# Kernel optimization log

Measured on AMD Instinct MI355X. Metric: run time of the kernel, lower is better.

## Reference

```python
import jax, jax.numpy as jnp
import numpy as np


def squash(v, axis=-1):
    # scale = |v|^2 / (1+|v|^2) / |v|, applied elementwise along `axis`
    s2 = jnp.sum(jnp.square(v), axis=axis, keepdims=True)
    scale = s2 / (1.0 + s2) / jnp.sqrt(s2)
    return scale * v


def setup_inputs() -> dict:
    key = jax.random.key(0)
    k1, k2 = jax.random.split(key)
    B, I, D_in = 128, 1152, 8   # batch, input_num_capsule, input_dim_vector
    N, D_out = 32, 16           # num_capsule, dim_vector
    inputs = jax.random.normal(k1, (B, I, D_in), dtype=jnp.float32)
    # glorot_uniform-like scale for W: [in_caps, num_caps, in_dim, out_dim]
    limit = np.sqrt(6.0 / (D_in + D_out)).astype(np.float32)
    W = jax.random.uniform(k2, (I, N, D_in, D_out), dtype=jnp.float32,
                           minval=-limit, maxval=limit)
    bias = jnp.zeros((1, I, N), dtype=jnp.float32)  # routing logits (zeros init)
    return {"inputs": inputs, "W": W, "bias": bias}


def reference(inputs, W, bias):
    num_routing = 3
    # inputs_hat[b,i,n,e] = sum_d inputs[b,i,d] * W[i,n,d,e]
    # (the original's tf.scan over batch + batch_dot is just this einsum)
    u_hat = jnp.einsum('bid,inde->bine', inputs, W)  # [B,I,N,E]

    b = jnp.broadcast_to(bias, u_hat.shape[:3])  # [B,I,N] (bias broadcasts over batch)
    outputs = None
    for it in range(num_routing):
        c = jax.nn.softmax(b, axis=2)                       # softmax over num_capsule
        s = jnp.einsum('bin,bine->bne', c, u_hat)           # weighted sum over in_caps
        outputs = squash(s, axis=-1)                        # [B,N,E]
        if it != num_routing - 1:
            # agreement update: b += <u_hat, v>
            b = b + jnp.einsum('bine,bne->bin', u_hat, outputs)
    return outputs  # [B, num_capsule, dim_vector]
```

## Files before the change

kernel.cpp:

```cpp
#include <hip/hip_runtime.h>
#include <hip/hip_fp16.h>

namespace {

constexpr int kB = 128, kI = 1152, kD = 8, kN = 32, kE = 16;
constexpr int kTI = 4;
constexpr int kNC = kI / kTI;
constexpr int kCG = 4;
constexpr int kCPG = kNC / kCG;

constexpr size_t kPartBytes = (size_t)kNC * kB * kN * kE * 2;
constexpr size_t kPart2Bytes = (size_t)kCG * kB * kN * kE * 4;
constexpr size_t kVsumBytes = (size_t)kB * kN * kE * 4;

typedef _Float16 h2v __attribute__((ext_vector_type(2)));

__device__ __forceinline__ float fdot2(__half2 a, __half2 b, float c) {
#if defined(__has_builtin) && __has_builtin(__builtin_amdgcn_fdot2)
  return __builtin_amdgcn_fdot2(__builtin_bit_cast(h2v, a),
                                __builtin_bit_cast(h2v, b), c, false);
#else
  float2 af = __half22float2(a), bf = __half22float2(b);
  return fmaf(af.y, bf.y, fmaf(af.x, bf.x, c));
#endif
}

union I4H { int4 v; __half2 h[4]; };

template<int PASS>
__global__ __launch_bounds__(256, 2)
void caps_pass(const float* __restrict__ x, const float* __restrict__ W,
               const float* __restrict__ bias, const __half* __restrict__ vsh,
               __half* __restrict__ part)
{
  __shared__ __half2 wlds[kTI * kD * 64 * 4];
  __shared__ __half2 xlds[32][kTI * kD];

  const int chunk = (int)blockIdx.x;
  const int i0 = chunk * kTI;
  const int b0 = (int)blockIdx.y * 32;
  const int t = (int)threadIdx.x;
  const int lane = t & 63;
  const int wv = t >> 6;
  const int eh = lane >> 5;
  const int n  = lane & 31;

  {
    const float2* wsrc = reinterpret_cast<const float2*>(
        W + (size_t)chunk * (kTI * kN * kD * kE));
    const int e  = (t * 2) & 15;
    const int dd = ((t * 2) >> 4) & 7;
    const int ehw = e >> 3, ep = (e & 7) >> 1;
#pragma unroll
    for (int iter = 0; iter < 32; ++iter) {
      const int nn_i = iter * 4 + (t >> 6);
      const int nn = nn_i & 31, ii = nn_i >> 5;
      float2 f2 = wsrc[iter * 256 + t];
      wlds[((ii * kD + dd) * 64 + ehw * 32 + nn) * 4 + ep] =
          __floats2half2_rn(f2.x, f2.y);
    }
  }
  {
    const int r = t >> 3, c = (t & 7) * 4;
    const float4 f4 = *reinterpret_cast<const float4*>(
        x + (size_t)(b0 + r) * (kI * kD) + i0 * kD + c);
    xlds[r][c + 0] = __half2half2(__float2half_rn(f4.x));
    xlds[r][c + 1] = __half2half2(__float2half_rn(f4.y));
    xlds[r][c + 2] = __half2half2(__float2half_rn(f4.z));
    xlds[r][c + 3] = __half2half2(__float2half_rn(f4.w));
  }
  __syncthreads();

  __half2 wr[kTI][kD][4];
#pragma unroll
  for (int i = 0; i < kTI; ++i)
#pragma unroll
    for (int d = 0; d < kD; ++d) {
      I4H q; q.v = *reinterpret_cast<const int4*>(&wlds[((i * kD + d) * 64 + lane) * 4]);
#pragma unroll
      for (int k = 0; k < 4; ++k) wr[i][d][k] = q.h[k];
    }

  float bf[kTI];
#pragma unroll
  for (int i = 0; i < kTI; ++i) bf[i] = bias[(size_t)(i0 + i) * kN + n];

  __half2 c0[kTI];
  if (PASS == 0) {
#pragma unroll
    for (int i = 0; i < kTI; ++i) {
      float lg = bf[i];
      float m = lg;
#pragma unroll
      for (int o = 1; o <= 16; o <<= 1) m = fmaxf(m, __shfl_xor(m, o, 64));
      float ev = __expf(lg - m);
      float sm = ev;
#pragma unroll
      for (int o = 1; o <= 16; o <<= 1) sm += __shfl_xor(sm, o, 64);
      c0[i] = __half2half2(__float2half_rn(ev / sm));
    }
  }

#pragma unroll 2
  for (int bb = 0; bb < 8; ++bb) {
    const int bl = wv * 8 + bb;
    const int b = b0 + bl;
    I4H vq;
    if (PASS > 0)
      vq.v = *reinterpret_cast<const int4*>(vsh + ((size_t)b * kN + n) * kE + eh * 8);

    __half2 s[4];
#pragma unroll
    for (int k = 0; k < 4; ++k) s[k] = __half2half2(__float2half(0.f));

#pragma unroll
    for (int i = 0; i < kTI; ++i) {
      I4H xa, xb;
      xa.v = *reinterpret_cast<const int4*>(&xlds[bl][i * kD]);
      xb.v = *reinterpret_cast<const int4*>(&xlds[bl][i * kD + 4]);
      __half2 uh[4];
#pragma unroll
      for (int k = 0; k < 4; ++k) uh[k] = __hmul2(xa.h[0], wr[i][0][k]);
#pragma unroll
      for (int d = 1; d < 4; ++d)
#pragma unroll
        for (int k = 0; k < 4; ++k) uh[k] = __hfma2(xa.h[d], wr[i][d][k], uh[k]);
#pragma unroll
      for (int d = 0; d < 4; ++d)
#pragma unroll
        for (int k = 0; k < 4; ++k) uh[k] = __hfma2(xb.h[d], wr[i][4 + d][k], uh[k]);

      __half2 c2;
      if (PASS == 0) {
        c2 = c0[i];
      } else {
        float lg = bf[i];
#pragma unroll
        for (int k = 0; k < 4; ++k) lg = fdot2(uh[k], vq.h[k], lg);
        lg += __shfl_xor(lg, 32, 64);
        float m = lg;
#pragma unroll
        for (int o = 1; o <= 16; o <<= 1) m = fmaxf(m, __shfl_xor(m, o, 64));
        float ev = __expf(lg - m);
        float sm = ev;
#pragma unroll
        for (int o = 1; o <= 16; o <<= 1) sm += __shfl_xor(sm, o, 64);
        c2 = __half2half2(__float2half_rn(ev / sm));
      }
#pragma unroll
      for (int k = 0; k < 4; ++k) s[k] = __hfma2(c2, uh[k], s[k]);
    }
    I4H o;
#pragma unroll
    for (int k = 0; k < 4; ++k) o.h[k] = s[k];
    *reinterpret_cast<int4*>(
        part + (((size_t)chunk * kB + b) * kN + n) * kE + eh * 8) = o.v;
  }
}

__global__ __launch_bounds__(256)
void caps_reduce1(const __half* __restrict__ part, float* __restrict__ partial2)
{
  const int b = (int)blockIdx.x, cg = (int)blockIdx.y;
  const int t = (int)threadIdx.x;
  const int nl = t >> 3, ep = t & 7;
  const __half2* p = reinterpret_cast<const __half2*>(
      part + (((size_t)(cg * kCPG) * kB + b) * kN + nl) * kE + ep * 2);
  const size_t stride = (size_t)kB * kN * kE / 2;
  float ax = 0.f, ay = 0.f;
#pragma unroll 8
  for (int ch = 0; ch < kCPG; ++ch) {
    float2 f = __half22float2(p[(size_t)ch * stride]);
    ax += f.x; ay += f.y;
  }
  *reinterpret_cast<float2*>(
      partial2 + (((size_t)cg * kB + b) * kN + nl) * kE + ep * 2) = make_float2(ax, ay);
}

template<int MODE>
__global__ __launch_bounds__(256)
void caps_final(const float* __restrict__ partial2, float* __restrict__ vsum,
                __half* __restrict__ vsh, float* __restrict__ out)
{
  const int b = (int)blockIdx.x;
  const int t = (int)threadIdx.x;
  const int nl = t >> 3, ep = t & 7;
  const size_t o = ((size_t)b * kN + nl) * kE + ep * 2;
  float ax = 0.f, ay = 0.f;
#pragma unroll
  for (int cg = 0; cg < kCG; ++cg) {
    float2 f = *reinterpret_cast<const float2*>(
        partial2 + (size_t)cg * kB * kN * kE + o);
    ax += f.x; ay += f.y;
  }
  float s2 = ax * ax + ay * ay;
  s2 += __shfl_xor(s2, 1, 64);
  s2 += __shfl_xor(s2, 2, 64);
  s2 += __shfl_xor(s2, 4, 64);
  const float sc = (s2 / (1.f + s2)) * rsqrtf(fmaxf(s2, 1e-30f));
  float vx = ax * sc, vy = ay * sc;
  if (MODE == 2) {
    *reinterpret_cast<float2*>(out + o) = make_float2(vx, vy);
  } else {
    if (MODE == 1) {
      float2 old = *reinterpret_cast<const float2*>(vsum + o);
      vx += old.x; vy += old.y;
    }
    *reinterpret_cast<float2*>(vsum + o) = make_float2(vx, vy);
    *reinterpret_cast<__half2*>(vsh + o) = __floats2half2_rn(vx, vy);
  }
}

}

extern "C" void kernel_launch(void* const* d_in, const int* in_sizes, int n_in,
                              void* d_out, int out_size, void* d_ws, size_t ws_size,
                              hipStream_t stream) {
  (void)in_sizes; (void)n_in; (void)out_size; (void)ws_size;
  const float* x    = reinterpret_cast<const float*>(d_in[0]);
  const float* W    = reinterpret_cast<const float*>(d_in[1]);
  const float* bias = reinterpret_cast<const float*>(d_in[2]);
  float* out = reinterpret_cast<float*>(d_out);

  char* ws = reinterpret_cast<char*>(d_ws);
  __half* part     = reinterpret_cast<__half*>(ws);
  float*  partial2 = reinterpret_cast<float*>(ws + kPartBytes);
  float*  vsum     = reinterpret_cast<float*>(ws + kPartBytes + kPart2Bytes);
  __half* vsh      = reinterpret_cast<__half*>(ws + kPartBytes + kPart2Bytes + kVsumBytes);

  dim3 pg(kNC, kB / 32), pb(256);
  dim3 rg(kB, kCG), rb(256);

  caps_pass<0><<<pg, pb, 0, stream>>>(x, W, bias, vsh, part);
  caps_reduce1<<<rg, rb, 0, stream>>>(part, partial2);
  caps_final<0><<<kB, 256, 0, stream>>>(partial2, vsum, vsh, out);
  caps_pass<1><<<pg, pb, 0, stream>>>(x, W, bias, vsh, part);
  caps_reduce1<<<rg, rb, 0, stream>>>(part, partial2);
  caps_final<1><<<kB, 256, 0, stream>>>(partial2, vsum, vsh, out);
  caps_pass<2><<<pg, pb, 0, stream>>>(x, W, bias, vsh, part);
  caps_reduce1<<<rg, rb, 0, stream>>>(part, partial2);
  caps_final<2><<<kB, 256, 0, stream>>>(partial2, vsum, vsh, out);
}
```

Baseline: 204.9 us.

## Load W directly into registers and widen reduction loads to 16 bytes

The pass kernel drops the LDS staging buffer for W. Each thread now reads its own W slice from global memory straight into registers with float4 loads, which removes the shared-memory round trip and about 32 KB of LDS per block. The only barrier left guards the x tile. The reduce kernel is restructured so each thread accumulates 8 halves through 128-bit loads, with 4 batches per block and a quarter of the blocks. The risk is less coalesced W global reads, since lanes stride by n across 512 B rows.

```diff
diff --git a/kernel.cpp b/kernel.cpp
--- a/kernel.cpp
+++ b/kernel.cpp
@@ -9,9 +9,9 @@
 constexpr int kCG = 4;
 constexpr int kCPG = kNC / kCG;
 
-constexpr size_t kPartBytes = (size_t)kNC * kB * kN * kE * 2;
+constexpr size_t kPartBytes  = (size_t)kNC * kB * kN * kE * 2;
 constexpr size_t kPart2Bytes = (size_t)kCG * kB * kN * kE * 4;
-constexpr size_t kVsumBytes = (size_t)kB * kN * kE * 4;
+constexpr size_t kVsumBytes  = (size_t)kB * kN * kE * 4;
 
 typedef _Float16 h2v __attribute__((ext_vector_type(2)));
 
@@ -33,7 +33,6 @@
                const float* __restrict__ bias, const __half* __restrict__ vsh,
                __half* __restrict__ part)
 {
-  __shared__ __half2 wlds[kTI * kD * 64 * 4];
   __shared__ __half2 xlds[32][kTI * kD];
 
   const int chunk = (int)blockIdx.x;
@@ -46,40 +45,31 @@
   const int n  = lane & 31;
 
   {
-    const float2* wsrc = reinterpret_cast<const float2*>(
-        W + (size_t)chunk * (kTI * kN * kD * kE));
-    const int e  = (t * 2) & 15;
-    const int dd = ((t * 2) >> 4) & 7;
-    const int ehw = e >> 3, ep = (e & 7) >> 1;
-#pragma unroll
-    for (int iter = 0; iter < 32; ++iter) {
-      const int nn_i = iter * 4 + (t >> 6);
-      const int nn = nn_i & 31, ii = nn_i >> 5;
-      float2 f2 = wsrc[iter * 256 + t];
-      wlds[((ii * kD + dd) * 64 + ehw * 32 + nn) * 4 + ep] =
-          __floats2half2_rn(f2.x, f2.y);
-    }
-  }
-  {
     const int r = t >> 3, c = (t & 7) * 4;
     const float4 f4 = *reinterpret_cast<const float4*>(
-        x + (size_t)(b0 + r) * (kI * kD) + i0 * kD + c);
+        x + (size_t)(b0 + r) * (kI * kD) + (size_t)i0 * kD + c);
     xlds[r][c + 0] = __half2half2(__float2half_rn(f4.x));
     xlds[r][c + 1] = __half2half2(__float2half_rn(f4.y));
     xlds[r][c + 2] = __half2half2(__float2half_rn(f4.z));
     xlds[r][c + 3] = __half2half2(__float2half_rn(f4.w));
   }
-  __syncthreads();
 
   __half2 wr[kTI][kD][4];
-#pragma unroll
-  for (int i = 0; i < kTI; ++i)
-#pragma unroll
-    for (int d = 0; d < kD; ++d) {
-      I4H q; q.v = *reinterpret_cast<const int4*>(&wlds[((i * kD + d) * 64 + lane) * 4]);
-#pragma unroll
-      for (int k = 0; k < 4; ++k) wr[i][d][k] = q.h[k];
-    }
+  {
+    const float* wb = W + ((size_t)i0 * kN + n) * (kD * kE) + eh * 8;
+#pragma unroll
+    for (int i = 0; i < kTI; ++i)
+#pragma unroll
+      for (int d = 0; d < kD; ++d) {
+        const float4* p = reinterpret_cast<const float4*>(
+            wb + (size_t)i * (kN * kD * kE) + d * kE);
+        float4 a = p[0], b4 = p[1];
+        wr[i][d][0] = __floats2half2_rn(a.x, a.y);
+        wr[i][d][1] = __floats2half2_rn(a.z, a.w);
+        wr[i][d][2] = __floats2half2_rn(b4.x, b4.y);
+        wr[i][d][3] = __floats2half2_rn(b4.z, b4.w);
+      }
+  }
 
   float bf[kTI];
 #pragma unroll
@@ -100,6 +90,8 @@
       c0[i] = __half2half2(__float2half_rn(ev / sm));
     }
   }
+
+  __syncthreads();
 
 #pragma unroll 2
   for (int bb = 0; bb < 8; ++bb) {
@@ -161,20 +153,25 @@
 __global__ __launch_bounds__(256)
 void caps_reduce1(const __half* __restrict__ part, float* __restrict__ partial2)
 {
-  const int b = (int)blockIdx.x, cg = (int)blockIdx.y;
+  const int cg = (int)blockIdx.y;
   const int t = (int)threadIdx.x;
-  const int nl = t >> 3, ep = t & 7;
-  const __half2* p = reinterpret_cast<const __half2*>(
-      part + (((size_t)(cg * kCPG) * kB + b) * kN + nl) * kE + ep * 2);
-  const size_t stride = (size_t)kB * kN * kE / 2;
-  float ax = 0.f, ay = 0.f;
-#pragma unroll 8
+  const int b = (int)blockIdx.x * 4 + (t >> 6);
+  const int l = t & 63;
+  const __half* p0 = part + ((size_t)(cg * kCPG) * kB + b) * (kN * kE) + l * 8;
+  constexpr size_t chStride = (size_t)kB * kN * kE;
+  float acc[8] = {0.f, 0.f, 0.f, 0.f, 0.f, 0.f, 0.f, 0.f};
+#pragma unroll 4
   for (int ch = 0; ch < kCPG; ++ch) {
-    float2 f = __half22float2(p[(size_t)ch * stride]);
-    ax += f.x; ay += f.y;
-  }
-  *reinterpret_cast<float2*>(
-      partial2 + (((size_t)cg * kB + b) * kN + nl) * kE + ep * 2) = make_float2(ax, ay);
+    I4H q; q.v = *reinterpret_cast<const int4*>(p0 + (size_t)ch * chStride);
+#pragma unroll
+    for (int k = 0; k < 4; ++k) {
+      float2 f = __half22float2(q.h[k]);
+      acc[2 * k] += f.x; acc[2 * k + 1] += f.y;
+    }
+  }
+  float* dst = partial2 + ((size_t)cg * kB + b) * (kN * kE) + l * 8;
+  *reinterpret_cast<float4*>(dst)     = make_float4(acc[0], acc[1], acc[2], acc[3]);
+  *reinterpret_cast<float4*>(dst + 4) = make_float4(acc[4], acc[5], acc[6], acc[7]);
 }
 
 template<int MODE>
@@ -229,7 +226,7 @@
   __half* vsh      = reinterpret_cast<__half*>(ws + kPartBytes + kPart2Bytes + kVsumBytes);
 
   dim3 pg(kNC, kB / 32), pb(256);
-  dim3 rg(kB, kCG), rb(256);
+  dim3 rg(kB / 4, kCG), rb(256);
 
   caps_pass<0><<<pg, pb, 0, stream>>>(x, W, bias, vsh, part);
   caps_reduce1<<<rg, rb, 0, stream>>>(part, partial2);
```

Measured after the change: 255.4 us. 24.6% more time.
